# Kernel tuning notes

Hardware: AMD Instinct MI355X
Metric: run time of the kernel (lower is better)

## Reference

```python
import jax, jax.numpy as jnp
import numpy as np

N_BINS = 15


def setup_inputs() -> dict:
    key = jax.random.key(0)
    k1, k2 = jax.random.split(key)
    probs = jax.random.uniform(k1, (1, 2, 4096, 4096), dtype=jnp.float32)
    labels = jax.random.randint(k2, (1, 1, 4096, 4096), 0, 2, dtype=jnp.int32)
    return {"probs": probs, "labels": labels}


def _bin_stats(conf, acc, boundaries):
    # bin i holds conf in (boundaries[i], boundaries[i+1]] -> searchsorted left - 1
    idx = jnp.searchsorted(boundaries, conf, side="left") - 1
    valid = (idx >= 0) & (idx < N_BINS)
    idx = jnp.where(valid, idx, N_BINS)  # route invalid (conf==0) to overflow bin
    vmask = valid.astype(conf.dtype)
    count = jax.ops.segment_sum(vmask, idx, num_segments=N_BINS + 1)[:N_BINS]
    csum = jax.ops.segment_sum(conf * vmask, idx, num_segments=N_BINS + 1)[:N_BINS]
    asum = jax.ops.segment_sum(acc * vmask, idx, num_segments=N_BINS + 1)[:N_BINS]
    return count, csum, asum


def reference(probs, labels):
    h, w = probs.shape[2], probs.shape[3]
    boundaries = jnp.linspace(0.0, 1.0, N_BINS + 1)
    conf0 = probs[0, 0].reshape(h * w)
    conf1 = probs[0, 1].reshape(h * w)
    lab = labels[0, 0].reshape(h * w)
    acc0 = (lab == 0).astype(probs.dtype)
    acc1 = (lab == 1).astype(probs.dtype)
    count0, csum0, asum0 = _bin_stats(conf0, acc0, boundaries)
    count1, csum1, asum1 = _bin_stats(conf1, acc1, boundaries)
    return (count0, csum0, asum0, count1, csum1, asum1)
```

## Files before the change

### kernel.cpp

```cpp
#include <hip/hip_runtime.h>
#include <stdint.h>


#define NBINS 15

__global__ void zero_out_kernel(float* out, int n) {
    int i = blockIdx.x * blockDim.x + threadIdx.x;
    if (i < n) out[i] = 0.0f;
}

__device__ __forceinline__ unsigned long long pack_update(float c, int match, int* bin_out) {
    bool valid = (c > 0.0f) && (c <= 1.0f);
    float cb = fmaxf(fminf(c * 15.0f, 14.0f), 0.0f);
    *bin_out = (int)cb;
    unsigned int cf = __float2uint_rn(fmaxf(c, 0.0f) * 262144.0f);
    unsigned long long v = ((unsigned long long)cf << 32)
                         | ((unsigned long long)(match ? 1u : 0u) << 16)
                         | 1ull;
    return valid ? v : 0ull;
}

__global__ __launch_bounds__(256) void calib_hist_kernel(
        const float* __restrict__ probs, const int* __restrict__ labels,
        float* __restrict__ out, int npix) {
    __shared__ unsigned long long hist[32 * 256];
    int tid = threadIdx.x;
    #pragma unroll
    for (int k = 0; k < 32; ++k) hist[k * 256 + tid] = 0ull;
    __syncthreads();

    const float4* p0 = (const float4*)probs;
    const float4* p1 = (const float4*)(probs + npix);
    const int4*   lb = (const int4*)labels;
    int nvec   = npix >> 2;
    int stride = gridDim.x * blockDim.x;

    for (int i = blockIdx.x * blockDim.x + tid; i < nvec; i += stride) {
        float4 a = p0[i];
        float4 b = p1[i];
        int4   l = lb[i];
        int bin;
        unsigned long long v;
        v = pack_update(a.x, l.x == 0, &bin); hist[bin * 256 + tid] += v;
        v = pack_update(b.x, l.x == 1, &bin); hist[(16 + bin) * 256 + tid] += v;
        v = pack_update(a.y, l.y == 0, &bin); hist[bin * 256 + tid] += v;
        v = pack_update(b.y, l.y == 1, &bin); hist[(16 + bin) * 256 + tid] += v;
        v = pack_update(a.z, l.z == 0, &bin); hist[bin * 256 + tid] += v;
        v = pack_update(b.z, l.z == 1, &bin); hist[(16 + bin) * 256 + tid] += v;
        v = pack_update(a.w, l.w == 0, &bin); hist[bin * 256 + tid] += v;
        v = pack_update(b.w, l.w == 1, &bin); hist[(16 + bin) * 256 + tid] += v;
    }
    __syncthreads();

    if (tid < 32) {
        int e = tid;
        unsigned long long cnt = 0, asum = 0, csum = 0;
        for (int it = 0; it < 256; ++it) {
            int t = (it + e) & 255;
            unsigned long long x = hist[e * 256 + t];
            cnt  += x & 0xFFFFull;
            asum += (x >> 16) & 0xFFFFull;
            csum += x >> 32;
        }
        int ch = e >> 4, bin = e & 15;
        if (bin < NBINS) {
            float* base = out + ch * 45;
            atomicAdd(base + bin,             (float)cnt);
            atomicAdd(base + NBINS + bin,     (float)csum * (1.0f / 262144.0f));
            atomicAdd(base + 2 * NBINS + bin, (float)asum);
        }
    }
}

extern "C" void kernel_launch(void* const* d_in, const int* in_sizes, int n_in,
                              void* d_out, int out_size, void* d_ws, size_t ws_size,
                              hipStream_t stream) {
    const float* probs  = (const float*)d_in[0];
    const int*   labels = (const int*)d_in[1];
    float*       out    = (float*)d_out;
    int npix = in_sizes[1];

    zero_out_kernel<<<(out_size + 127) / 128, 128, 0, stream>>>(out, out_size);

    int nvec = npix >> 2;
    int blocks = (nvec + 256 * 32 - 1) / (256 * 32);
    if (blocks < 1) blocks = 1;
    calib_hist_kernel<<<blocks, 256, 0, stream>>>(probs, labels, out, npix);
}
```

Baseline: 258.1 us.

## Pack per-thread histogram into 32-bit words and parallelize the bin reduction

Shrinks each per-thread shared-memory histogram entry from 64 to 32 bits by quantizing confidence to 1/2048 with a 7-bit count and a 7-bit accuracy field. This halves LDS footprint and traffic and allows more resident blocks, declared via launch bounds. The main loop now prefetches the next vector before doing the histogram updates. The final reduction is spread over all 256 threads with shuffles, instead of 32 serial threads. The grid is doubled so each thread handles fewer items, which keeps the narrow fields from overflowing. The cost is a coarser confidence quantization in csum.

```diff
diff --git a/kernel.cpp b/kernel.cpp
--- a/kernel.cpp
+++ b/kernel.cpp
@@ -9,24 +9,26 @@
     if (i < n) out[i] = 0.0f;
 }
 
-__device__ __forceinline__ unsigned long long pack_update(float c, int match, int* bin_out) {
+__device__ __forceinline__ unsigned pack_u32(float c, int match, int* bin_out) {
     bool valid = (c > 0.0f) && (c <= 1.0f);
     float cb = fmaxf(fminf(c * 15.0f, 14.0f), 0.0f);
     *bin_out = (int)cb;
-    unsigned int cf = __float2uint_rn(fmaxf(c, 0.0f) * 262144.0f);
-    unsigned long long v = ((unsigned long long)cf << 32)
-                         | ((unsigned long long)(match ? 1u : 0u) << 16)
-                         | 1ull;
-    return valid ? v : 0ull;
+    unsigned cf = __float2uint_rn(fmaxf(c, 0.0f) * 2048.0f);
+    unsigned v = (cf << 14) | ((match ? 1u : 0u) << 7) | 1u;
+    return valid ? v : 0u;
 }
 
-__global__ __launch_bounds__(256) void calib_hist_kernel(
+__global__ __launch_bounds__(256, 4) void calib_hist_kernel(
         const float* __restrict__ probs, const int* __restrict__ labels,
         float* __restrict__ out, int npix) {
-    __shared__ unsigned long long hist[32 * 256];
+    __shared__ unsigned histA[16 * 256];
+    __shared__ unsigned histB[16 * 256];
     int tid = threadIdx.x;
     #pragma unroll
-    for (int k = 0; k < 32; ++k) hist[k * 256 + tid] = 0ull;
+    for (int k = 0; k < 16; ++k) {
+        histA[k * 256 + tid] = 0u;
+        histB[k * 256 + tid] = 0u;
+    }
     __syncthreads();
 
     const float4* p0 = (const float4*)probs;
@@ -35,39 +37,52 @@
     int nvec   = npix >> 2;
     int stride = gridDim.x * blockDim.x;
 
-    for (int i = blockIdx.x * blockDim.x + tid; i < nvec; i += stride) {
-        float4 a = p0[i];
-        float4 b = p1[i];
+    int i = blockIdx.x * blockDim.x + tid;
+    if (i < nvec) {
+        float4 a = p0[i], b = p1[i];
         int4   l = lb[i];
-        int bin;
-        unsigned long long v;
-        v = pack_update(a.x, l.x == 0, &bin); hist[bin * 256 + tid] += v;
-        v = pack_update(b.x, l.x == 1, &bin); hist[(16 + bin) * 256 + tid] += v;
-        v = pack_update(a.y, l.y == 0, &bin); hist[bin * 256 + tid] += v;
-        v = pack_update(b.y, l.y == 1, &bin); hist[(16 + bin) * 256 + tid] += v;
-        v = pack_update(a.z, l.z == 0, &bin); hist[bin * 256 + tid] += v;
-        v = pack_update(b.z, l.z == 1, &bin); hist[(16 + bin) * 256 + tid] += v;
-        v = pack_update(a.w, l.w == 0, &bin); hist[bin * 256 + tid] += v;
-        v = pack_update(b.w, l.w == 1, &bin); hist[(16 + bin) * 256 + tid] += v;
+        while (true) {
+            int  ni   = i + stride;
+            bool more = ni < nvec;
+            float4 a2, b2; int4 l2;
+            if (more) { a2 = p0[ni]; b2 = p1[ni]; l2 = lb[ni]; }
+            int bin; unsigned v;
+            v = pack_u32(a.x, l.x == 0, &bin); histA[bin * 256 + tid] += v;
+            v = pack_u32(b.x, l.x == 1, &bin); histB[bin * 256 + tid] += v;
+            v = pack_u32(a.y, l.y == 0, &bin); histA[bin * 256 + tid] += v;
+            v = pack_u32(b.y, l.y == 1, &bin); histB[bin * 256 + tid] += v;
+            v = pack_u32(a.z, l.z == 0, &bin); histA[bin * 256 + tid] += v;
+            v = pack_u32(b.z, l.z == 1, &bin); histB[bin * 256 + tid] += v;
+            v = pack_u32(a.w, l.w == 0, &bin); histA[bin * 256 + tid] += v;
+            v = pack_u32(b.w, l.w == 1, &bin); histB[bin * 256 + tid] += v;
+            if (!more) break;
+            i = ni; a = a2; b = b2; l = l2;
+        }
     }
     __syncthreads();
 
-    if (tid < 32) {
-        int e = tid;
-        unsigned long long cnt = 0, asum = 0, csum = 0;
-        for (int it = 0; it < 256; ++it) {
-            int t = (it + e) & 255;
-            unsigned long long x = hist[e * 256 + t];
-            cnt  += x & 0xFFFFull;
-            asum += (x >> 16) & 0xFFFFull;
-            csum += x >> 32;
+    {
+        int h   = tid;
+        int e   = h >> 3, ch = e >> 4, bin = e & 15;
+        const unsigned* src = ch ? histB : histA;
+        unsigned cnt = 0, asum = 0, csum = 0;
+        int base = (h & 7) * 32;
+        #pragma unroll
+        for (int j = 0; j < 32; ++j) {
+            int col = base + ((j + h) & 31);
+            unsigned x = src[bin * 256 + col];
+            cnt  += x & 0x7Fu;
+            asum += (x >> 7) & 0x7Fu;
+            csum += x >> 14;
         }
-        int ch = e >> 4, bin = e & 15;
-        if (bin < NBINS) {
-            float* base = out + ch * 45;
-            atomicAdd(base + bin,             (float)cnt);
-            atomicAdd(base + NBINS + bin,     (float)csum * (1.0f / 262144.0f));
-            atomicAdd(base + 2 * NBINS + bin, (float)asum);
+        cnt  += __shfl_xor(cnt, 1); asum += __shfl_xor(asum, 1); csum += __shfl_xor(csum, 1);
+        cnt  += __shfl_xor(cnt, 2); asum += __shfl_xor(asum, 2); csum += __shfl_xor(csum, 2);
+        cnt  += __shfl_xor(cnt, 4); asum += __shfl_xor(asum, 4); csum += __shfl_xor(csum, 4);
+        if ((h & 7) == 0 && bin < NBINS) {
+            float* obase = out + ch * 45;
+            atomicAdd(obase + bin,               (float)cnt);
+            atomicAdd(obase + NBINS + bin,       (float)csum * (1.0f / 2048.0f));
+            atomicAdd(obase + 2 * NBINS + bin,   (float)asum);
         }
     }
 }
@@ -83,7 +98,7 @@
     zero_out_kernel<<<(out_size + 127) / 128, 128, 0, stream>>>(out, out_size);
 
     int nvec = npix >> 2;
-    int blocks = (nvec + 256 * 32 - 1) / (256 * 32);
+    int blocks = (nvec + 256 * 16 - 1) / (256 * 16);
     if (blocks < 1) blocks = 1;
     calib_hist_kernel<<<blocks, 256, 0, stream>>>(probs, labels, out, npix);
 }
```

Measured after the change: 292.6 us. 13.3% more time.
